# Optimization experiments

Hardware: AMD Instinct MI355X
Metric: run time of the kernel (lower is better)

## Reference

```python
import jax, jax.numpy as jnp
import numpy as np

B, IN, OUT, G = 8192, 512, 512, 20


def setup_inputs() -> dict:
    key = jax.random.key(0)
    k1, k2, k3 = jax.random.split(key, 3)
    x = jax.random.normal(k1, (B, IN), dtype=jnp.float32)
    coeffs = jax.random.normal(k2, (OUT, IN, G + 1), dtype=jnp.float32) * 0.1
    base_w = jax.random.normal(k3, (OUT, IN), dtype=jnp.float32) * 0.1
    return {"x": x, "coeffs": coeffs, "base_w": base_w}


def reference(x, coeffs, base_w):
    g = coeffs.shape[-1] - 1  # grid_size
    xc = jnp.clip(x, -1.0, 1.0)
    base = jax.nn.silu(xc) @ base_w.T  # [B, out]
    x_grid = (xc + 1.0) * 0.5 * g  # [B, in], in [0, g]
    idx = jnp.clip(jnp.floor(x_grid).astype(jnp.int32), 0, g - 1)  # [B, in]
    t = x_grid - idx.astype(x.dtype)  # [B, in]
    b, n = x.shape
    bi = jnp.arange(b)[:, None]
    fi = jnp.arange(n)[None, :]
    # Sparse interpolation weights over grid bins: 2 nonzeros per (b, i).
    w = jnp.zeros((b, n, g + 1), dtype=x.dtype)
    w = w.at[bi, fi, idx].add(1.0 - t)
    w = w.at[bi, fi, idx + 1].add(t)  # idx+1 <= g since idx <= g-1
    # y[b,o] = sum_i sum_g w[b,i,g] * coeffs[o,i,g]
    y = jnp.einsum('big,oig->bo', w, coeffs)
    return base + y
```

## Files before the change

kernel.cpp:

```cpp
#include <hip/hip_runtime.h>
#include <stdint.h>


typedef short v8s __attribute__((ext_vector_type(8)));
typedef float v4f __attribute__((ext_vector_type(4)));

#define B_DIM 8192
#define IN_DIM 512
#define OUT_DIM 512
#define G_DIM 20
#define SLOTS 24
#define FPT 4
#define KT_TOTAL (IN_DIM / FPT)
#define KSPLIT 4
#define KT_PER (KT_TOTAL / KSPLIT)
#define BM 128
#define BN 128
#define CHUNKS 12
#define PLANE 2048
#define TILE_BYTES (CHUNKS * PLANE)

#define P_BYTES ((size_t)IN_DIM * B_DIM * 8)
#define WT_BYTES ((size_t)(OUT_DIM / BN) * KT_TOTAL * TILE_BYTES)
#define PART_ELEMS ((size_t)B_DIM * OUT_DIM)
#define WS_NEED (P_BYTES + WT_BYTES + (size_t)KSPLIT * PART_ELEMS * 4)

#define PACK_BLKS ((B_DIM / 64) * (IN_DIM / 64))
#define WPACK_BLKS ((OUT_DIM * IN_DIM) / 256)

static __device__ __forceinline__ unsigned f2bf(float f) {
  unsigned u = __builtin_bit_cast(unsigned, f);
  return (u + 0x7fffu + ((u >> 16) & 1u)) >> 16;
}

static __device__ __forceinline__ void load16(const void* g, void* l) {
  __builtin_amdgcn_global_load_lds(
      (const __attribute__((address_space(1))) unsigned*)g,
      (__attribute__((address_space(3))) unsigned*)l, 16, 0, 0);
}

__global__ void zero_out_kernel(uint4* __restrict__ out) {
  out[(size_t)blockIdx.x * 256 + threadIdx.x] = uint4{0u, 0u, 0u, 0u};
}

__global__ void pack_fused_kernel(const float* __restrict__ x, uint2* __restrict__ P,
                                  const float* __restrict__ coeffs,
                                  const float* __restrict__ base_w,
                                  char* __restrict__ Wt) {
  __shared__ uint2 tile[64 * 65];
  const int t = threadIdx.x;
  if (blockIdx.x < PACK_BLKS) {
    const int b0 = (blockIdx.x & (B_DIM / 64 - 1)) * 64;
    const int i0 = (blockIdx.x / (B_DIM / 64)) * 64;
    const int tr = t >> 6;
    const int tc = t & 63;
#pragma unroll
    for (int it = 0; it < 16; ++it) {
      int br = it * 4 + tr;
      float xv = x[(size_t)(b0 + br) * IN_DIM + i0 + tc];
      float xc = fminf(fmaxf(xv, -1.0f), 1.0f);
      float xg = (xc + 1.0f) * 10.0f;
      int idx = (int)floorf(xg);
      idx = idx < 0 ? 0 : (idx > G_DIM - 1 ? G_DIM - 1 : idx);
      float tt = xg - (float)idx;
      float sl = xc / (1.0f + __expf(-xc));
      uint2 pv;
      pv.x = f2bf(1.0f - tt) | (f2bf(tt) << 16);
      pv.y = (unsigned)idx | (f2bf(sl) << 16);
      tile[tc * 65 + br] = pv;
    }
    __syncthreads();
#pragma unroll
    for (int it = 0; it < 16; ++it) {
      int ir = it * 4 + tr;
      P[(size_t)(i0 + ir) * B_DIM + b0 + tc] = tile[ir * 65 + tc];
    }
  } else {
    const unsigned u = (blockIdx.x - PACK_BLKS) * 256 + t;
    const int s = u >> 9;
    const int w = u & 511;
    const int row = w >> 2;
    const int f = w & 3;
    const int n_blk = s / KT_TOTAL;
    const int kt = s - n_blk * KT_TOTAL;
    const int o = n_blk * 128 + row;
    const int i = kt * 4 + f;
    const size_t g = (size_t)o * IN_DIM + i;
    const float* c = coeffs + g * 21;
    float cf[21];
#pragma unroll
    for (int j = 0; j < 21; ++j) cf[j] = c[j];
    float bw = base_w[g];
    unsigned d[12];
#pragma unroll
    for (int j = 0; j < 10; ++j) d[j] = f2bf(cf[2 * j]) | (f2bf(cf[2 * j + 1]) << 16);
    d[10] = f2bf(cf[20]) | (f2bf(bw) << 16);
    d[11] = 0u;
    char* slab = Wt + (size_t)s * TILE_BYTES;
#pragma unroll
    for (int p = 0; p < 3; ++p)
      *(uint4*)(slab + (3 * f + p) * PLANE + row * 16) =
          uint4{d[4 * p], d[4 * p + 1], d[4 * p + 2], d[4 * p + 3]};
  }
}

__global__ void reduce_kernel(const v4f* __restrict__ p, v4f* __restrict__ out) {
  size_t i = (size_t)blockIdx.x * 256 + threadIdx.x;
  const size_t q = PART_ELEMS / 4;
  v4f a = p[i], b = p[i + q], c = p[i + 2 * q], d = p[i + 3 * q];
  out[i] = (a + b) + (c + d);
}

static __device__ __forceinline__ void build_strip(uint2 pv, unsigned d[12]) {
  const unsigned w0w1 = pv.x;
  const unsigned w0hi = pv.x << 16;
  const unsigned w1lo = pv.x >> 16;
  const int idx = (int)(pv.y & 0xffffu);
  const unsigned slhi = pv.y & 0xffff0000u;
#pragma unroll
  for (int q = 0; q <= 10; ++q) {
    unsigned v = 0u;
    v = (idx == 2 * q - 1) ? w1lo : v;
    v = (idx == 2 * q)     ? w0w1 : v;
    v = (idx == 2 * q + 1) ? w0hi : v;
    d[q] = v;
  }
  d[10] |= slhi;
  d[11] = 0u;
}

template <bool ATOMIC>
__global__ __launch_bounds__(256, 3) void kan_gemm(const uint2* __restrict__ P,
                                                   const char* __restrict__ Wt,
                                                   float* __restrict__ dst) {
  __shared__ uint4 lds4[(2 * TILE_BYTES) / 16];
  char* Ab = (char*)lds4;
  char* Bb = (char*)lds4 + TILE_BYTES;
  const int t = threadIdx.x;
  const int lane = t & 63;
  const int wv = t >> 6;
  const int wm = wv >> 1, wn = wv & 1;
  const int b0 = blockIdx.x * BM;
  const int n_blk = blockIdx.y;
  const int kt0 = blockIdx.z * KT_PER;
  const int ktend = kt0 + KT_PER;

  v4f acc[4][4];
  const v4f z4 = {0.f, 0.f, 0.f, 0.f};
#pragma unroll
  for (int ii = 0; ii < 4; ++ii)
#pragma unroll
    for (int jj = 0; jj < 4; ++jj) acc[ii][jj] = z4;

  uint2 pv0 = P[(size_t)(kt0 * 4 + wv) * B_DIM + b0 + lane];
  uint2 pv1 = P[(size_t)(kt0 * 4 + wv) * B_DIM + b0 + lane + 64];

  const int r16 = lane & 15;
  const int q16 = lane >> 4;

  for (int kt = kt0; kt < ktend; ++kt) {
    __syncthreads();

    const char* wsrc = Wt + (size_t)(n_blk * KT_TOTAL + kt) * TILE_BYTES;
#pragma unroll
    for (int q = 0; q < 6; ++q)
      load16(wsrc + (q * 256 + t) * 16, Bb + (q * 256 + t) * 16);

    const int ktn = (kt + 1 < ktend) ? kt + 1 : kt;
    uint2 pn0 = P[(size_t)(ktn * 4 + wv) * B_DIM + b0 + lane];
    uint2 pn1 = P[(size_t)(ktn * 4 + wv) * B_DIM + b0 + lane + 64];

    unsigned d[12];
    build_strip(pv0, d);
#pragma unroll
    for (int p = 0; p < 3; ++p)
      *(uint4*)(Ab + (3 * wv + p) * PLANE + lane * 16) =
          uint4{d[4 * p], d[4 * p + 1], d[4 * p + 2], d[4 * p + 3]};
    build_strip(pv1, d);
#pragma unroll
    for (int p = 0; p < 3; ++p)
      *(uint4*)(Ab + (3 * wv + p) * PLANE + (lane + 64) * 16) =
          uint4{d[4 * p], d[4 * p + 1], d[4 * p + 2], d[4 * p + 3]};
    pv0 = pn0;
    pv1 = pn1;

    __syncthreads();

#pragma unroll
    for (int s = 0; s < 3; ++s) {
      const int chunk = s * 4 + q16;
      v8s af[4], bfr[4];
#pragma unroll
      for (int rm = 0; rm < 4; ++rm) {
        int row = wm * 64 + rm * 16 + r16;
        af[rm] = *(const v8s*)(Ab + chunk * PLANE + row * 16);
      }
#pragma unroll
      for (int cn = 0; cn < 4; ++cn) {
        int row = wn * 64 + cn * 16 + r16;
        bfr[cn] = *(const v8s*)(Bb + chunk * PLANE + row * 16);
      }
#pragma unroll
      for (int rm = 0; rm < 4; ++rm)
#pragma unroll
        for (int cn = 0; cn < 4; ++cn)
          acc[rm][cn] = __builtin_amdgcn_mfma_f32_16x16x32_bf16(af[rm], bfr[cn], acc[rm][cn], 0, 0, 0);
    }
  }

  float* o = ATOMIC ? dst : dst + (size_t)blockIdx.z * PART_ELEMS;
  const int q4 = (lane >> 4) * 4;
#pragma unroll
  for (int rm = 0; rm < 4; ++rm)
#pragma unroll
    for (int cn = 0; cn < 4; ++cn)
#pragma unroll
      for (int r = 0; r < 4; ++r) {
        int row = b0 + wm * 64 + rm * 16 + q4 + r;
        int col = n_blk * BN + wn * 64 + cn * 16 + r16;
        if (ATOMIC)
          atomicAdd(o + (size_t)row * OUT_DIM + col, acc[rm][cn][r]);
        else
          o[(size_t)row * OUT_DIM + col] = acc[rm][cn][r];
      }
}

extern "C" void kernel_launch(void* const* d_in, const int* in_sizes, int n_in,
                              void* d_out, int out_size, void* d_ws, size_t ws_size,
                              hipStream_t stream) {
  const float* x = (const float*)d_in[0];
  const float* coeffs = (const float*)d_in[1];
  const float* base_w = (const float*)d_in[2];
  float* out = (float*)d_out;

  uint2* P = (uint2*)d_ws;
  char* Wt = (char*)d_ws + P_BYTES;
  float* part = (float*)((char*)d_ws + P_BYTES + WT_BYTES);

  pack_fused_kernel<<<PACK_BLKS + WPACK_BLKS, 256, 0, stream>>>(x, P, coeffs, base_w, Wt);

  if (ws_size >= WS_NEED) {
    kan_gemm<false><<<dim3(B_DIM / BM, OUT_DIM / BN, KSPLIT), 256, 0, stream>>>(P, Wt, part);
    reduce_kernel<<<(int)(PART_ELEMS / 4 / 256), 256, 0, stream>>>((const v4f*)part, (v4f*)out);
  } else {
    zero_out_kernel<<<(int)((PART_ELEMS * 4) / 4096), 256, 0, stream>>>((uint4*)out);
    kan_gemm<true><<<dim3(B_DIM / BM, OUT_DIM / BN, KSPLIT), 256, 0, stream>>>(P, Wt, out);
  }
}
```

Baseline: 209.9 us.

## Fuse split-K reduction into GEMM via ticket counter and use three K splits

Removes the separate reduce kernel. Each GEMM block writes its partial tile, then bumps a per-tile ticket counter, and the last block to arrive sums the other partials with its own accumulators and writes the output. The split count drops from 4 to 3 with uneven K ranges, which cuts partial-buffer traffic and the grid size. Tickets are zeroed in the pack kernel. The cost is threadfence/atomic synchronisation and a serialized tail in the last-arriving blocks.

Result: slower. 316.4 us (+50.7%).

```diff
diff --git a/kernel.cpp b/kernel.cpp
--- a/kernel.cpp
+++ b/kernel.cpp
@@ -9,21 +9,20 @@
 #define IN_DIM 512
 #define OUT_DIM 512
 #define G_DIM 20
-#define SLOTS 24
 #define FPT 4
 #define KT_TOTAL (IN_DIM / FPT)
-#define KSPLIT 4
-#define KT_PER (KT_TOTAL / KSPLIT)
+#define KSPLIT 3
 #define BM 128
 #define BN 128
 #define CHUNKS 12
 #define PLANE 2048
 #define TILE_BYTES (CHUNKS * PLANE)
+#define NTILES ((B_DIM / BM) * (OUT_DIM / BN))
 
 #define P_BYTES ((size_t)IN_DIM * B_DIM * 8)
 #define WT_BYTES ((size_t)(OUT_DIM / BN) * KT_TOTAL * TILE_BYTES)
 #define PART_ELEMS ((size_t)B_DIM * OUT_DIM)
-#define WS_NEED (P_BYTES + WT_BYTES + (size_t)KSPLIT * PART_ELEMS * 4)
+#define WS_NEED (P_BYTES + WT_BYTES + (size_t)KSPLIT * PART_ELEMS * 4 + NTILES * 4)
 
 #define PACK_BLKS ((B_DIM / 64) * (IN_DIM / 64))
 #define WPACK_BLKS ((OUT_DIM * IN_DIM) / 256)
@@ -46,7 +45,8 @@
 __global__ void pack_fused_kernel(const float* __restrict__ x, uint2* __restrict__ P,
                                   const float* __restrict__ coeffs,
                                   const float* __restrict__ base_w,
-                                  char* __restrict__ Wt) {
+                                  char* __restrict__ Wt,
+                                  unsigned* __restrict__ ticket) {
   __shared__ uint2 tile[64 * 65];
   const int t = threadIdx.x;
   if (blockIdx.x < PACK_BLKS) {
@@ -77,6 +77,7 @@
     }
   } else {
     const unsigned u = (blockIdx.x - PACK_BLKS) * 256 + t;
+    if (u < NTILES) ticket[u] = 0u;
     const int s = u >> 9;
     const int w = u & 511;
     const int row = w >> 2;
@@ -104,13 +105,6 @@
   }
 }
 
-__global__ void reduce_kernel(const v4f* __restrict__ p, v4f* __restrict__ out) {
-  size_t i = (size_t)blockIdx.x * 256 + threadIdx.x;
-  const size_t q = PART_ELEMS / 4;
-  v4f a = p[i], b = p[i + q], c = p[i + 2 * q], d = p[i + 3 * q];
-  out[i] = (a + b) + (c + d);
-}
-
 static __device__ __forceinline__ void build_strip(uint2 pv, unsigned d[12]) {
   const unsigned w0w1 = pv.x;
   const unsigned w0hi = pv.x << 16;
@@ -132,8 +126,11 @@
 template <bool ATOMIC>
 __global__ __launch_bounds__(256, 3) void kan_gemm(const uint2* __restrict__ P,
                                                    const char* __restrict__ Wt,
-                                                   float* __restrict__ dst) {
+                                                   float* __restrict__ part,
+                                                   float* __restrict__ out,
+                                                   unsigned* __restrict__ ticket) {
   __shared__ uint4 lds4[(2 * TILE_BYTES) / 16];
+  __shared__ unsigned last_flag;
   char* Ab = (char*)lds4;
   char* Bb = (char*)lds4 + TILE_BYTES;
   const int t = threadIdx.x;
@@ -142,8 +139,9 @@
   const int wm = wv >> 1, wn = wv & 1;
   const int b0 = blockIdx.x * BM;
   const int n_blk = blockIdx.y;
-  const int kt0 = blockIdx.z * KT_PER;
-  const int ktend = kt0 + KT_PER;
+  const int z = blockIdx.z;
+  const int kt0 = (z * KT_TOTAL) / KSPLIT;
+  const int ktend = ((z + 1) * KT_TOTAL) / KSPLIT;
 
   v4f acc[4][4];
   const v4f z4 = {0.f, 0.f, 0.f, 0.f};
@@ -208,8 +206,22 @@
     }
   }
 
-  float* o = ATOMIC ? dst : dst + (size_t)blockIdx.z * PART_ELEMS;
   const int q4 = (lane >> 4) * 4;
+  if (ATOMIC) {
+#pragma unroll
+    for (int rm = 0; rm < 4; ++rm)
+#pragma unroll
+      for (int cn = 0; cn < 4; ++cn)
+#pragma unroll
+        for (int r = 0; r < 4; ++r) {
+          int row = b0 + wm * 64 + rm * 16 + q4 + r;
+          int col = n_blk * BN + wn * 64 + cn * 16 + r16;
+          atomicAdd(out + (size_t)row * OUT_DIM + col, acc[rm][cn][r]);
+        }
+    return;
+  }
+
+  float* mypart = part + (size_t)z * PART_ELEMS;
 #pragma unroll
   for (int rm = 0; rm < 4; ++rm)
 #pragma unroll
@@ -218,11 +230,29 @@
       for (int r = 0; r < 4; ++r) {
         int row = b0 + wm * 64 + rm * 16 + q4 + r;
         int col = n_blk * BN + wn * 64 + cn * 16 + r16;
-        if (ATOMIC)
-          atomicAdd(o + (size_t)row * OUT_DIM + col, acc[rm][cn][r]);
-        else
-          o[(size_t)row * OUT_DIM + col] = acc[rm][cn][r];
+        mypart[(size_t)row * OUT_DIM + col] = acc[rm][cn][r];
       }
+  __threadfence();
+  __syncthreads();
+  if (t == 0)
+    last_flag = (atomicAdd(&ticket[n_blk * (B_DIM / BM) + blockIdx.x], 1u) == KSPLIT - 1);
+  __syncthreads();
+  if (last_flag) {
+    __threadfence();
+    const float* pa = part + (size_t)((z + 1) % KSPLIT) * PART_ELEMS;
+    const float* pb = part + (size_t)((z + 2) % KSPLIT) * PART_ELEMS;
+#pragma unroll
+    for (int rm = 0; rm < 4; ++rm)
+#pragma unroll
+      for (int cn = 0; cn < 4; ++cn)
+#pragma unroll
+        for (int r = 0; r < 4; ++r) {
+          int row = b0 + wm * 64 + rm * 16 + q4 + r;
+          int col = n_blk * BN + wn * 64 + cn * 16 + r16;
+          size_t off = (size_t)row * OUT_DIM + col;
+          out[off] = acc[rm][cn][r] + pa[off] + pb[off];
+        }
+  }
 }
 
 extern "C" void kernel_launch(void* const* d_in, const int* in_sizes, int n_in,
@@ -236,14 +266,15 @@
   uint2* P = (uint2*)d_ws;
   char* Wt = (char*)d_ws + P_BYTES;
   float* part = (float*)((char*)d_ws + P_BYTES + WT_BYTES);
-
-  pack_fused_kernel<<<PACK_BLKS + WPACK_BLKS, 256, 0, stream>>>(x, P, coeffs, base_w, Wt);
+  unsigned* ticket = (unsigned*)((char*)d_ws + P_BYTES + WT_BYTES +
+                                 (size_t)KSPLIT * PART_ELEMS * 4);
+
+  pack_fused_kernel<<<PACK_BLKS + WPACK_BLKS, 256, 0, stream>>>(x, P, coeffs, base_w, Wt, ticket);
 
   if (ws_size >= WS_NEED) {
-    kan_gemm<false><<<dim3(B_DIM / BM, OUT_DIM / BN, KSPLIT), 256, 0, stream>>>(P, Wt, part);
-    reduce_kernel<<<(int)(PART_ELEMS / 4 / 256), 256, 0, stream>>>((const v4f*)part, (v4f*)out);
+    kan_gemm<false><<<dim3(B_DIM / BM, OUT_DIM / BN, KSPLIT), 256, 0, stream>>>(P, Wt, part, out, ticket);
   } else {
     zero_out_kernel<<<(int)((PART_ELEMS * 4) / 4096), 256, 0, stream>>>((uint4*)out);
-    kan_gemm<true><<<dim3(B_DIM / BM, OUT_DIM / BN, KSPLIT), 256, 0, stream>>>(P, Wt, out);
-  }
-}
+    kan_gemm<true><<<dim3(B_DIM / BM, OUT_DIM / BN, KSPLIT), 256, 0, stream>>>(P, Wt, part, out, ticket);
+  }
+}
```
